# Kernel optimization log

Hardware: AMD Instinct MI355X
Metric: run time of the kernel (lower is better)

Reference implementation:

```python
import jax, jax.numpy as jnp
import numpy as np

NUM_FEATS = 100000
EMB_DIM = 64
ATT_DIM = 64


def setup_inputs() -> dict:
    key = jax.random.key(0)
    ks = jax.random.split(key, 9)
    B, F = 2048, 39
    feat_index = jax.random.randint(ks[0], (B, F), 0, NUM_FEATS)
    feat_value = jax.random.uniform(ks[1], (B, F), dtype=jnp.float32)
    # parameters
    fo_w = jax.random.normal(ks[2], (NUM_FEATS, 1), dtype=jnp.float32) * 0.01
    emb_table = jax.random.normal(ks[3], (NUM_FEATS, EMB_DIM), dtype=jnp.float32) * 0.01
    att_W = jax.random.normal(ks[4], (EMB_DIM, ATT_DIM), dtype=jnp.float32) * (1.0 / np.sqrt(EMB_DIM))
    att_b = jax.random.normal(ks[5], (ATT_DIM,), dtype=jnp.float32)
    att_h = jax.random.normal(ks[6], (ATT_DIM,), dtype=jnp.float32)
    p_vec = jax.random.normal(ks[7], (EMB_DIM,), dtype=jnp.float32)
    bias = jax.random.normal(ks[8], (), dtype=jnp.float32)
    return {"feat_index": feat_index, "feat_value": feat_value, "fo_w": fo_w,
            "emb_table": emb_table, "att_W": att_W, "att_b": att_b,
            "att_h": att_h, "p_vec": p_vec, "bias": bias}


def _cross_indices(num_fields):
    row, col = np.triu_indices(num_fields, k=1)
    return jnp.asarray(row), jnp.asarray(col)


def reference(feat_index, feat_value, fo_w, emb_table, att_W, att_b, att_h, p_vec, bias):
    B, F = feat_index.shape
    fv = feat_value[:, :, None]                      # [B,F,1]
    # first-order term
    y_first = jnp.sum(fo_w[feat_index] * fv, axis=1)[:, 0]   # [B]
    # embeddings scaled by values
    feat_emb = emb_table[feat_index] * fv            # [B,F,D]
    row, col = _cross_indices(F)
    inter = feat_emb[:, row] * feat_emb[:, col]      # [B,P,D], P=F*(F-1)/2
    # location-based attention
    sig = jax.nn.relu(jnp.einsum('bpd,da->bpa', inter, att_W) + att_b)
    sig = jnp.sum(sig * att_h, axis=2)               # [B,P]
    att = jax.nn.softmax(sig, axis=1)                # [B,P]
    pooled = jnp.einsum('bp,bpd->bd', att, inter)    # [B,D]
    att_pool = jnp.sum(pooled * p_vec, axis=1)       # [B]
    y = jax.nn.sigmoid(bias + y_first + att_pool)    # [B]
    return y
```

## Files before the change

### kernel.cpp

```cpp
#include <hip/hip_runtime.h>
#include <hip/hip_fp16.h>

#define NUM_F  39
#define NUM_P  741
#define NPAD   768
#define DIM    64
#define ESTRH  72
#define NRP    2
#define NITEMS (2 * NUM_F * 8)

typedef float    f32x4 __attribute__((ext_vector_type(4)));
typedef _Float16 f16x8 __attribute__((ext_vector_type(8)));
typedef _Float16 f16x2 __attribute__((ext_vector_type(2)));
typedef __fp16   h16x2 __attribute__((ext_vector_type(2)));

static __device__ __forceinline__ f16x8 pack8(float4 v0, float4 v1, float fv) {
    f16x8 hv;
    hv[0] = (_Float16)(v0.x * fv);
    hv[1] = (_Float16)(v0.y * fv);
    hv[2] = (_Float16)(v0.z * fv);
    hv[3] = (_Float16)(v0.w * fv);
    hv[4] = (_Float16)(v1.x * fv);
    hv[5] = (_Float16)(v1.y * fv);
    hv[6] = (_Float16)(v1.z * fv);
    hv[7] = (_Float16)(v1.w * fv);
    return hv;
}

static __device__ __forceinline__ f16x2 pk2(float a, float b) {
    union { h16x2 p; f16x2 v; } u;
    u.p = __builtin_amdgcn_cvt_pkrtz(a, b);
    return u.v;
}
static __device__ __forceinline__ f16x2 relu2(f16x2 x) {
#if __has_builtin(__builtin_elementwise_max)
    const f16x2 z = {(_Float16)0.f, (_Float16)0.f};
    return __builtin_elementwise_max(x, z);
#else
    f16x2 r;
    r[0] = (x[0] > (_Float16)0.f) ? x[0] : (_Float16)0.f;
    r[1] = (x[1] > (_Float16)0.f) ? x[1] : (_Float16)0.f;
    return r;
#endif
}

__global__ __launch_bounds__(512, 4) void afm_pp2(
    const int*   __restrict__ feat_index,
    const float* __restrict__ feat_value,
    const float* __restrict__ fo_w,
    const float* __restrict__ emb_table,
    const float* __restrict__ att_W,
    const float* __restrict__ att_b,
    const float* __restrict__ att_h,
    const float* __restrict__ p_vec,
    const float* __restrict__ bias,
    float*       __restrict__ out)
{
    const int blk  = blockIdx.x;
    const int t    = threadIdx.x;
    const int wave = t >> 6;
    const int lane = t & 63;
    const int row  = wave >> 2;
    const int wv   = wave & 3;
    const int la   = lane & 15;
    const int lg   = lane >> 4;

    __shared__ __half       e_lds[2][2][NUM_F][ESTRH];
    __shared__ __half       Wt[DIM][ESTRH];
    __shared__ float2       sq_s[2][NPAD];
    __shared__ float        b_lds[DIM], h_lds[DIM], pv_lds[DIM];
    __shared__ unsigned int pairOff[NPAD];
    __shared__ int          s_idx[2 * NRP * NUM_F];
    __shared__ float        s_fv[2 * NRP * NUM_F];
    __shared__ float        yf_s[2 * NRP * NUM_F];
    __shared__ float        s_yfirst[2 * NRP];
    __shared__ float        wredM[8], wredS[8], wredQ[8];

    const float4* emb4 = (const float4*)emb_table;

    if (t < 2 * NRP * NUM_F) {
        int   idx = feat_index[blk * 2 * NRP * NUM_F + t];
        float fv  = feat_value[blk * 2 * NRP * NUM_F + t];
        s_idx[t]  = idx;
        s_fv[t]   = fv;
        yf_s[t]   = fo_w[idx] * fv;
    }
    if (t < DIM) {
        b_lds[t]  = att_b[t];
        h_lds[t]  = att_h[t];
        pv_lds[t] = p_vec[t];
    }
    if (t >= 192 && t < 192 + NUM_F) {
        int r = t - 192, off = r * (2 * NUM_F - r - 1) / 2;
        const unsigned int rb = (unsigned int)(r * (ESTRH * 2));
        for (int c = r + 1; c < NUM_F; ++c) {
            pairOff[off] = rb | ((unsigned int)(c * (ESTRH * 2)) << 16);
            ++off;
        }
    }
    if (t >= 256 && t < 256 + (NPAD - NUM_P)) pairOff[NUM_P + (t - 256)] = 0;
    for (int q = t; q < DIM * DIM; q += 512) {
        int d = q >> 6, a = q & 63;
        Wt[a][d] = (__half)(_Float16)att_W[q];
    }
    __syncthreads();

    if (wave < 2 * NRP) {
        float yf = (lane < NUM_F) ? yf_s[wave * NUM_F + lane] : 0.f;
        #pragma unroll
        for (int m = 1; m < 64; m <<= 1) yf += __shfl_xor(yf, m);
        if (lane == 0) s_yfirst[wave] = yf;
    }

    {
        const int f0 = t >> 3, d80 = t & 7;
        float4 v0a = emb4[(size_t)s_idx[f0] * 16 + d80 * 2];
        float4 v0b = emb4[(size_t)s_idx[f0] * 16 + d80 * 2 + 1];
        const int  i1   = t + 512;
        const bool has1 = i1 < NITEMS;
        const int  f1 = i1 >> 3, d81 = i1 & 7;
        float4 v1a, v1b;
        if (has1) {
            v1a = emb4[(size_t)s_idx[f1] * 16 + d81 * 2];
            v1b = emb4[(size_t)s_idx[f1] * 16 + d81 * 2 + 1];
        }
        {
            int rr = (f0 >= NUM_F), ff = f0 - rr * NUM_F;
            *(f16x8*)&e_lds[0][rr][ff][d80 * 8] = pack8(v0a, v0b, s_fv[f0]);
        }
        if (has1) {
            int rr = (f1 >= NUM_F), ff = f1 - rr * NUM_F;
            *(f16x8*)&e_lds[0][rr][ff][d81 * 8] = pack8(v1a, v1b, s_fv[f1]);
        }
    }
    __syncthreads();

    const f16x8 WA00 = *(const f16x8*)&Wt[ 0 + la][ 0 + lg * 8];
    const f16x8 WA01 = *(const f16x8*)&Wt[ 0 + la][32 + lg * 8];
    const f16x8 WA10 = *(const f16x8*)&Wt[16 + la][ 0 + lg * 8];
    const f16x8 WA11 = *(const f16x8*)&Wt[16 + la][32 + lg * 8];
    const f16x8 WA20 = *(const f16x8*)&Wt[32 + la][ 0 + lg * 8];
    const f16x8 WA21 = *(const f16x8*)&Wt[32 + la][32 + lg * 8];
    const f16x8 WA30 = *(const f16x8*)&Wt[48 + la][ 0 + lg * 8];
    const f16x8 WA31 = *(const f16x8*)&Wt[48 + la][32 + lg * 8];

    f16x8 PA0 = (f16x8)(_Float16)0.f;
    f16x8 PA1 = (f16x8)(_Float16)0.f;
    if (la == 0) {
        #pragma unroll
        for (int j = 0; j < 8; ++j) {
            PA0[j] = (_Float16)pv_lds[     lg * 8 + j];
            PA1[j] = (_Float16)pv_lds[32 + lg * 8 + j];
        }
    }

    const f32x4 b40 = *(const f32x4*)&b_lds[ 0 + lg * 4];
    const f32x4 b41 = *(const f32x4*)&b_lds[16 + lg * 4];
    const f32x4 b42 = *(const f32x4*)&b_lds[32 + lg * 4];
    const f32x4 b43 = *(const f32x4*)&b_lds[48 + lg * 4];
    const f16x2 h20 = pk2(h_lds[ 0 + lg * 4], h_lds[ 0 + lg * 4 + 1]);
    const f16x2 h21 = pk2(h_lds[ 0 + lg * 4 + 2], h_lds[ 0 + lg * 4 + 3]);
    const f16x2 h22 = pk2(h_lds[16 + lg * 4], h_lds[16 + lg * 4 + 1]);
    const f16x2 h23 = pk2(h_lds[16 + lg * 4 + 2], h_lds[16 + lg * 4 + 3]);
    const f16x2 h24 = pk2(h_lds[32 + lg * 4], h_lds[32 + lg * 4 + 1]);
    const f16x2 h25 = pk2(h_lds[32 + lg * 4 + 2], h_lds[32 + lg * 4 + 3]);
    const f16x2 h26 = pk2(h_lds[48 + lg * 4], h_lds[48 + lg * 4 + 1]);
    const f16x2 h27 = pk2(h_lds[48 + lg * 4 + 2], h_lds[48 + lg * 4 + 3]);
    const f32x4 z4  = {0.f, 0.f, 0.f, 0.f};

    const int lgo = lg * 16;

    for (int rp = 0; rp < NRP; ++rp) {
        float4 n0a, n0b, n1a, n1b;
        int    nf0 = 0, nd0 = 0, nf1 = 0, nd1 = 0;
        bool   nhas1 = false;
        if (rp + 1 < NRP) {
            const int off = (rp + 1) * 2 * NUM_F;
            nf0 = t >> 3; nd0 = t & 7;
            n0a = emb4[(size_t)s_idx[off + nf0] * 16 + nd0 * 2];
            n0b = emb4[(size_t)s_idx[off + nf0] * 16 + nd0 * 2 + 1];
            const int i1 = t + 512;
            nhas1 = i1 < NITEMS;
            nf1 = i1 >> 3; nd1 = i1 & 7;
            if (nhas1) {
                n1a = emb4[(size_t)s_idx[off + nf1] * 16 + nd1 * 2];
                n1b = emb4[(size_t)s_idx[off + nf1] * 16 + nd1 * 2 + 1];
            }
        }

        const char* e_base = (const char*)&e_lds[rp & 1][row][0][0];

        #pragma unroll 1
        for (int it = 0; it < 12; ++it) {
            const int tile = wv + it * 4;
            const int p    = (tile << 4) + la;
            const unsigned rc = pairOff[p];
            const unsigned ro = rc & 0xFFFFu;
            const unsigned co = rc >> 16;

            const f16x8 er0 = *(const f16x8*)(e_base + ro + lgo);
            const f16x8 er1 = *(const f16x8*)(e_base + ro + lgo + 64);
            const f16x8 ec0 = *(const f16x8*)(e_base + co + lgo);
            const f16x8 ec1 = *(const f16x8*)(e_base + co + lgo + 64);
            const f16x8 B0 = er0 * ec0;
            const f16x8 B1 = er1 * ec1;

            __builtin_amdgcn_s_setprio(1);
            f32x4 a0 = __builtin_amdgcn_mfma_f32_16x16x32_f16(WA00, B0, b40, 0, 0, 0);
            f32x4 a1 = __builtin_amdgcn_mfma_f32_16x16x32_f16(WA10, B0, b41, 0, 0, 0);
            f32x4 a2 = __builtin_amdgcn_mfma_f32_16x16x32_f16(WA20, B0, b42, 0, 0, 0);
            f32x4 a3 = __builtin_amdgcn_mfma_f32_16x16x32_f16(WA30, B0, b43, 0, 0, 0);
            f32x4 aq = __builtin_amdgcn_mfma_f32_16x16x32_f16(PA0,  B0, z4,  0, 0, 0);
            a0 = __builtin_amdgcn_mfma_f32_16x16x32_f16(WA01, B1, a0, 0, 0, 0);
            a1 = __builtin_amdgcn_mfma_f32_16x16x32_f16(WA11, B1, a1, 0, 0, 0);
            a2 = __builtin_amdgcn_mfma_f32_16x16x32_f16(WA21, B1, a2, 0, 0, 0);
            a3 = __builtin_amdgcn_mfma_f32_16x16x32_f16(WA31, B1, a3, 0, 0, 0);
            aq = __builtin_amdgcn_mfma_f32_16x16x32_f16(PA1,  B1, aq, 0, 0, 0);
            __builtin_amdgcn_s_setprio(0);

            f16x2 fa = relu2(pk2(a0[0], a0[1])) * h20;
            f16x2 fb = relu2(pk2(a0[2], a0[3])) * h21;
            fa = relu2(pk2(a1[0], a1[1])) * h22 + fa;
            fb = relu2(pk2(a1[2], a1[3])) * h23 + fb;
            fa = relu2(pk2(a2[0], a2[1])) * h24 + fa;
            fb = relu2(pk2(a2[2], a2[3])) * h25 + fb;
            fa = relu2(pk2(a3[0], a3[1])) * h26 + fa;
            fb = relu2(pk2(a3[2], a3[3])) * h27 + fb;
            const f16x2 fs = fa + fb;
            float ts = (float)fs[0] + (float)fs[1];
            ts += __shfl_xor(ts, 16);
            ts += __shfl_xor(ts, 32);

            if (lg == 0 && p < NUM_P) {
                sq_s[row][p] = make_float2(ts, aq[0]);
            }
        }
        __syncthreads();

        const int t2 = wv * 64 + lane;
        float sv0, sv1, sv2, qv0, qv1, qv2;
        {
            float2 x0 = sq_s[row][t2];
            float2 x1 = sq_s[row][t2 + 256];
            bool ok2 = (t2 + 512) < NUM_P;
            float2 x2 = ok2 ? sq_s[row][t2 + 512] : make_float2(-1e30f, 0.f);
            sv0 = x0.x; qv0 = x0.y;
            sv1 = x1.x; qv1 = x1.y;
            sv2 = x2.x; qv2 = x2.y;
            if (t2 + 256 >= NUM_P) { sv1 = -1e30f; qv1 = 0.f; }
            if (t2 >= NUM_P)       { sv0 = -1e30f; qv0 = 0.f; }
        }

        float m3 = fmaxf(fmaxf(sv0, sv1), sv2);
        #pragma unroll
        for (int mm = 1; mm < 64; mm <<= 1) m3 = fmaxf(m3, __shfl_xor(m3, mm));
        if (lane == 0) wredM[wave] = m3;
        __syncthreads();
        const int r4 = row * 4;
        const float M = fmaxf(fmaxf(wredM[r4 + 0], wredM[r4 + 1]),
                              fmaxf(wredM[r4 + 2], wredM[r4 + 3]));

        float e0 = __expf(sv0 - M);
        float e1 = __expf(sv1 - M);
        float e2 = __expf(sv2 - M);
        float S  = e0 + e1 + e2;
        float Q  = fmaf(e0, qv0, fmaf(e1, qv1, e2 * qv2));
        #pragma unroll
        for (int mm = 1; mm < 64; mm <<= 1) {
            S += __shfl_xor(S, mm);
            Q += __shfl_xor(Q, mm);
        }
        if (lane == 0) { wredS[wave] = S; wredQ[wave] = Q; }
        __syncthreads();

        if (lane == 0 && wv == 0) {
            const float Ssum = wredS[r4] + wredS[r4 + 1] + wredS[r4 + 2] + wredS[r4 + 3];
            const float Qsum = wredQ[r4] + wredQ[r4 + 1] + wredQ[r4 + 2] + wredQ[r4 + 3];
            const float att_pool = Qsum / Ssum;
            const float x = bias[0] + s_yfirst[rp * 2 + row] + att_pool;
            out[blk * (2 * NRP) + rp * 2 + row] = 1.f / (1.f + __expf(-x));
        }

        if (rp + 1 < NRP) {
            const int off = (rp + 1) * 2 * NUM_F;
            {
                int rr = (nf0 >= NUM_F), ff = nf0 - rr * NUM_F;
                *(f16x8*)&e_lds[(rp + 1) & 1][rr][ff][nd0 * 8] =
                    pack8(n0a, n0b, s_fv[off + nf0]);
            }
            if (nhas1) {
                int rr = (nf1 >= NUM_F), ff = nf1 - rr * NUM_F;
                *(f16x8*)&e_lds[(rp + 1) & 1][rr][ff][nd1 * 8] =
                    pack8(n1a, n1b, s_fv[off + nf1]);
            }
            __syncthreads();
        }
    }
}

extern "C" void kernel_launch(void* const* d_in, const int* in_sizes, int n_in,
                              void* d_out, int out_size, void* d_ws, size_t ws_size,
                              hipStream_t stream) {
    const int*   feat_index = (const int*)  d_in[0];
    const float* feat_value = (const float*)d_in[1];
    const float* fo_w       = (const float*)d_in[2];
    const float* emb_table  = (const float*)d_in[3];
    const float* att_W      = (const float*)d_in[4];
    const float* att_b      = (const float*)d_in[5];
    const float* att_h      = (const float*)d_in[6];
    const float* p_vec      = (const float*)d_in[7];
    const float* bias       = (const float*)d_in[8];
    float*       out        = (float*)d_out;

    const int B = in_sizes[0] / NUM_F;

    afm_pp2<<<B / (2 * NRP), 512, 0, stream>>>(feat_index, feat_value, fo_w, emb_table,
                                               att_W, att_b, att_h, p_vec, bias, out);
}
```

Measured before the change: 25.60 us.

## Software-pipeline LDS pair loads and replace p_vec MFMA with packed dot

The LDS reads of the row and column embeddings for the next pair tile are issued one iteration ahead, so they overlap the current tile's MFMAs. The p_vec projection moves from two MFMAs, which used only one lane row, to packed fp16 FMAs on the vector ALU. Its reduction is combined with the attention score into one packed-half cross-lane shuffle, which halves the shuffles. The cost is more register pressure from the double-buffered operands, and the score sum now accumulates in fp16 rather than fp32, which may lose precision.

```diff
diff --git a/kernel.cpp b/kernel.cpp
--- a/kernel.cpp
+++ b/kernel.cpp
@@ -43,8 +43,14 @@
     return r;
 #endif
 }
-
-__global__ __launch_bounds__(512, 4) void afm_pp2(
+static __device__ __forceinline__ f16x2 shflxor_add2(f16x2 v, int mask) {
+    union { f16x2 h; int i; } u, r;
+    u.h = v;
+    r.i = __shfl_xor(u.i, mask);
+    return v + r.h;
+}
+
+__global__ __launch_bounds__(512, 4) void afm_pp3(
     const int*   __restrict__ feat_index,
     const float* __restrict__ feat_value,
     const float* __restrict__ fo_w,
@@ -144,16 +150,6 @@
     const f16x8 WA30 = *(const f16x8*)&Wt[48 + la][ 0 + lg * 8];
     const f16x8 WA31 = *(const f16x8*)&Wt[48 + la][32 + lg * 8];
 
-    f16x8 PA0 = (f16x8)(_Float16)0.f;
-    f16x8 PA1 = (f16x8)(_Float16)0.f;
-    if (la == 0) {
-        #pragma unroll
-        for (int j = 0; j < 8; ++j) {
-            PA0[j] = (_Float16)pv_lds[     lg * 8 + j];
-            PA1[j] = (_Float16)pv_lds[32 + lg * 8 + j];
-        }
-    }
-
     const f32x4 b40 = *(const f32x4*)&b_lds[ 0 + lg * 4];
     const f32x4 b41 = *(const f32x4*)&b_lds[16 + lg * 4];
     const f32x4 b42 = *(const f32x4*)&b_lds[32 + lg * 4];
@@ -166,7 +162,14 @@
     const f16x2 h25 = pk2(h_lds[32 + lg * 4 + 2], h_lds[32 + lg * 4 + 3]);
     const f16x2 h26 = pk2(h_lds[48 + lg * 4], h_lds[48 + lg * 4 + 1]);
     const f16x2 h27 = pk2(h_lds[48 + lg * 4 + 2], h_lds[48 + lg * 4 + 3]);
-    const f32x4 z4  = {0.f, 0.f, 0.f, 0.f};
+    const f16x2 pvA0 = pk2(pv_lds[lg * 8 + 0], pv_lds[lg * 8 + 1]);
+    const f16x2 pvA1 = pk2(pv_lds[lg * 8 + 2], pv_lds[lg * 8 + 3]);
+    const f16x2 pvA2 = pk2(pv_lds[lg * 8 + 4], pv_lds[lg * 8 + 5]);
+    const f16x2 pvA3 = pk2(pv_lds[lg * 8 + 6], pv_lds[lg * 8 + 7]);
+    const f16x2 pvB0 = pk2(pv_lds[32 + lg * 8 + 0], pv_lds[32 + lg * 8 + 1]);
+    const f16x2 pvB1 = pk2(pv_lds[32 + lg * 8 + 2], pv_lds[32 + lg * 8 + 3]);
+    const f16x2 pvB2 = pk2(pv_lds[32 + lg * 8 + 4], pv_lds[32 + lg * 8 + 5]);
+    const f16x2 pvB3 = pk2(pv_lds[32 + lg * 8 + 6], pv_lds[32 + lg * 8 + 7]);
 
     const int lgo = lg * 16;
 
@@ -190,33 +193,56 @@
 
         const char* e_base = (const char*)&e_lds[rp & 1][row][0][0];
 
+        unsigned rc_nxt = pairOff[((wv + 4) << 4) + la];
+        f16x8 er0, er1, ec0, ec1;
+        {
+            const unsigned rc = pairOff[(wv << 4) + la];
+            const unsigned ro = rc & 0xFFFFu;
+            const unsigned co = rc >> 16;
+            er0 = *(const f16x8*)(e_base + ro + lgo);
+            er1 = *(const f16x8*)(e_base + ro + lgo + 64);
+            ec0 = *(const f16x8*)(e_base + co + lgo);
+            ec1 = *(const f16x8*)(e_base + co + lgo + 64);
+        }
+
         #pragma unroll 1
         for (int it = 0; it < 12; ++it) {
             const int tile = wv + it * 4;
             const int p    = (tile << 4) + la;
-            const unsigned rc = pairOff[p];
-            const unsigned ro = rc & 0xFFFFu;
-            const unsigned co = rc >> 16;
-
-            const f16x8 er0 = *(const f16x8*)(e_base + ro + lgo);
-            const f16x8 er1 = *(const f16x8*)(e_base + ro + lgo + 64);
-            const f16x8 ec0 = *(const f16x8*)(e_base + co + lgo);
-            const f16x8 ec1 = *(const f16x8*)(e_base + co + lgo + 64);
+
             const f16x8 B0 = er0 * ec0;
             const f16x8 B1 = er1 * ec1;
+
+            if (it < 11) {
+                const unsigned rc = rc_nxt;
+                if (it < 10) rc_nxt = pairOff[((wv + (it + 2) * 4) << 4) + la];
+                const unsigned ro = rc & 0xFFFFu;
+                const unsigned co = rc >> 16;
+                er0 = *(const f16x8*)(e_base + ro + lgo);
+                er1 = *(const f16x8*)(e_base + ro + lgo + 64);
+                ec0 = *(const f16x8*)(e_base + co + lgo);
+                ec1 = *(const f16x8*)(e_base + co + lgo + 64);
+            }
 
             __builtin_amdgcn_s_setprio(1);
             f32x4 a0 = __builtin_amdgcn_mfma_f32_16x16x32_f16(WA00, B0, b40, 0, 0, 0);
             f32x4 a1 = __builtin_amdgcn_mfma_f32_16x16x32_f16(WA10, B0, b41, 0, 0, 0);
             f32x4 a2 = __builtin_amdgcn_mfma_f32_16x16x32_f16(WA20, B0, b42, 0, 0, 0);
             f32x4 a3 = __builtin_amdgcn_mfma_f32_16x16x32_f16(WA30, B0, b43, 0, 0, 0);
-            f32x4 aq = __builtin_amdgcn_mfma_f32_16x16x32_f16(PA0,  B0, z4,  0, 0, 0);
             a0 = __builtin_amdgcn_mfma_f32_16x16x32_f16(WA01, B1, a0, 0, 0, 0);
             a1 = __builtin_amdgcn_mfma_f32_16x16x32_f16(WA11, B1, a1, 0, 0, 0);
             a2 = __builtin_amdgcn_mfma_f32_16x16x32_f16(WA21, B1, a2, 0, 0, 0);
             a3 = __builtin_amdgcn_mfma_f32_16x16x32_f16(WA31, B1, a3, 0, 0, 0);
-            aq = __builtin_amdgcn_mfma_f32_16x16x32_f16(PA1,  B1, aq, 0, 0, 0);
             __builtin_amdgcn_s_setprio(0);
+
+            f16x2 q2 = __builtin_shufflevector(B0, B0, 0, 1) * pvA0;
+            q2 = __builtin_shufflevector(B0, B0, 2, 3) * pvA1 + q2;
+            q2 = __builtin_shufflevector(B0, B0, 4, 5) * pvA2 + q2;
+            q2 = __builtin_shufflevector(B0, B0, 6, 7) * pvA3 + q2;
+            q2 = __builtin_shufflevector(B1, B1, 0, 1) * pvB0 + q2;
+            q2 = __builtin_shufflevector(B1, B1, 2, 3) * pvB1 + q2;
+            q2 = __builtin_shufflevector(B1, B1, 4, 5) * pvB2 + q2;
+            q2 = __builtin_shufflevector(B1, B1, 6, 7) * pvB3 + q2;
 
             f16x2 fa = relu2(pk2(a0[0], a0[1])) * h20;
             f16x2 fb = relu2(pk2(a0[2], a0[3])) * h21;
@@ -227,12 +253,15 @@
             fa = relu2(pk2(a3[0], a3[1])) * h26 + fa;
             fb = relu2(pk2(a3[2], a3[3])) * h27 + fb;
             const f16x2 fs = fa + fb;
-            float ts = (float)fs[0] + (float)fs[1];
-            ts += __shfl_xor(ts, 16);
-            ts += __shfl_xor(ts, 32);
+
+            f16x2 tq;
+            tq[0] = fs[0] + fs[1];
+            tq[1] = q2[0] + q2[1];
+            tq = shflxor_add2(tq, 16);
+            tq = shflxor_add2(tq, 32);
 
             if (lg == 0 && p < NUM_P) {
-                sq_s[row][p] = make_float2(ts, aq[0]);
+                sq_s[row][p] = make_float2((float)tq[0], (float)tq[1]);
             }
         }
         __syncthreads();
@@ -314,6 +343,6 @@
 
     const int B = in_sizes[0] / NUM_F;
 
-    afm_pp2<<<B / (2 * NRP), 512, 0, stream>>>(feat_index, feat_value, fo_w, emb_table,
+    afm_pp3<<<B / (2 * NRP), 512, 0, stream>>>(feat_index, feat_value, fo_w, emb_table,
                                                att_W, att_b, att_h, p_vec, bias, out);
 }
```

New measurement: 33.26 us. 29.9% more time.
